# Optimization experiments

Measured on AMD Instinct MI355X. Metric: run time of the kernel, lower is better.

Reference implementation:

```python
import jax, jax.numpy as jnp
import numpy as np

B, S, D, H = 1, 2048, 1024, 16
HD = D // H
FF = 4 * D
EPS_LN = 1e-5
EPS_ATTN = 1e-6


def _layernorm(x, g, b):
    mu = jnp.mean(x, axis=-1, keepdims=True)
    var = jnp.mean(jnp.square(x - mu), axis=-1, keepdims=True)
    return (x - mu) * jax.lax.rsqrt(var + EPS_LN) * g + b


def setup_inputs() -> dict:
    key = jax.random.key(0)
    ks = jax.random.split(key, 12)
    w = lambda k, shape: (jax.random.normal(k, shape, jnp.float32) * 0.02)
    return {
        "x": jax.random.normal(ks[0], (B, S, D), jnp.float32),
        "Wq": w(ks[1], (D, D)), "bq": jnp.zeros((D,), jnp.float32),
        "Wk": w(ks[2], (D, D)), "bk": jnp.zeros((D,), jnp.float32),
        "Wv": w(ks[3], (D, D)), "bv": jnp.zeros((D,), jnp.float32),
        "Wo": w(ks[4], (D, D)), "bo": jnp.zeros((D,), jnp.float32),
        "W1": w(ks[5], (FF, D)), "bb1": jnp.zeros((FF,), jnp.float32),
        "W2": w(ks[6], (D, FF)), "bb2": jnp.zeros((D,), jnp.float32),
        "g1": jnp.ones((D,), jnp.float32), "be1": jnp.zeros((D,), jnp.float32),
        "g2": jnp.ones((D,), jnp.float32), "be2": jnp.zeros((D,), jnp.float32),
    }


def reference(x, Wq, bq, Wk, bk, Wv, bv, Wo, bo, W1, bb1, W2, bb2, g1, be1, g2, be2):
    # --- pre-norm causal linear attention ---
    h = _layernorm(x, g1, be1)                     # (B,S,D)
    def heads(t):
        return t.reshape(B, S, H, HD).transpose(0, 2, 1, 3)  # (B,H,S,hd)
    q = heads(h @ Wq.T + bq)
    k = heads(h @ Wk.T + bk)
    v = heads(h @ Wv.T + bv)
    # feature map phi(x) = elu(x) + 1 (strictly positive)
    q = jax.nn.elu(q) + 1.0
    k = jax.nn.elu(k) + 1.0
    # causal cumulative state: S_t = sum_{i<=t} k_i v_i^T ; z_t = sum_{i<=t} k_i
    kv = jnp.cumsum(jnp.einsum("bhsd,bhse->bhsde", k, v), axis=2)  # (B,H,S,hd,hd)
    z = jnp.cumsum(k, axis=2)                                       # (B,H,S,hd)
    num = jnp.einsum("bhsd,bhsde->bhse", q, kv)                    # (B,H,S,hd)
    den = jnp.einsum("bhsd,bhsd->bhs", q, z) + EPS_ATTN
    attn = (num / den[..., None]).transpose(0, 2, 1, 3).reshape(B, S, D)
    attn = attn @ Wo.T + bo
    x = x + attn
    # --- FFN (GELU exact, matching torch nn.GELU default) ---
    h2 = _layernorm(x, g2, be2)
    ff = jax.nn.gelu(h2 @ W1.T + bb1, approximate=False) @ W2.T + bb2
    return x + ff
```

## Files before the change

kernel.cpp:

```cpp
#include <hip/hip_runtime.h>
#include <hip/hip_bf16.h>
#include <math.h>

constexpr int S  = 2048;
constexpr int D  = 1024;
constexpr int H  = 16;
constexpr int HD = 64;
constexpr int FF = 4096;
constexpr int NC  = 32;
constexpr int CHK = 64;
constexpr int QS  = 3 * D;

typedef __attribute__((ext_vector_type(8))) short bf16x8;
typedef __attribute__((ext_vector_type(4))) float f32x4;
typedef __attribute__((ext_vector_type(16))) float f32x16;

__device__ inline unsigned short f2bf(float f) {
    unsigned int u = __float_as_uint(f);
    u = (u + 0x7FFFu + ((u >> 16) & 1u)) >> 16;
    return (unsigned short)u;
}

constexpr int DD4 = D * D / 4;
constexpr int FD4 = FF * D / 4;
constexpr int CVT_TOTAL4 = 4 * DD4 + 2 * FD4;
constexpr int CVT_BLOCKS = CVT_TOTAL4 / 256;

__global__ __launch_bounds__(256) void cvt_ln(const float* __restrict__ x,
                                              const float* __restrict__ g,
                                              const float* __restrict__ b,
                                              unsigned short* __restrict__ lnout,
                                              const float* __restrict__ Wq,
                                              const float* __restrict__ Wk,
                                              const float* __restrict__ Wv,
                                              const float* __restrict__ Wo,
                                              const float* __restrict__ W1,
                                              const float* __restrict__ W2,
                                              unsigned short* __restrict__ Wqkvb,
                                              unsigned short* __restrict__ Wob,
                                              unsigned short* __restrict__ W1b,
                                              unsigned short* __restrict__ W2b) {
    const int tid = threadIdx.x;
    if (blockIdx.x >= S) {
        int i = (blockIdx.x - S) * 256 + tid;
        const float* s;
        unsigned short* dp;
        if (i < DD4)                 { s = Wq + (size_t)i * 4;               dp = Wqkvb + (size_t)i * 4; }
        else if (i < 2 * DD4)        { s = Wk + (size_t)(i - DD4) * 4;       dp = Wqkvb + (size_t)i * 4; }
        else if (i < 3 * DD4)        { s = Wv + (size_t)(i - 2 * DD4) * 4;   dp = Wqkvb + (size_t)i * 4; }
        else if (i < 4 * DD4)        { s = Wo + (size_t)(i - 3 * DD4) * 4;   dp = Wob + (size_t)(i - 3 * DD4) * 4; }
        else if (i < 4 * DD4 + FD4)  { s = W1 + (size_t)(i - 4 * DD4) * 4;   dp = W1b + (size_t)(i - 4 * DD4) * 4; }
        else                         { s = W2 + (size_t)(i - 4 * DD4 - FD4) * 4; dp = W2b + (size_t)(i - 4 * DD4 - FD4) * 4; }
        float4 v = *(const float4*)s;
        ushort4 o = { f2bf(v.x), f2bf(v.y), f2bf(v.z), f2bf(v.w) };
        *(ushort4*)dp = o;
        return;
    }
    const int row = blockIdx.x;
    float4 v = ((const float4*)(x + (size_t)row * D))[tid];
    float s  = v.x + v.y + v.z + v.w;
    float ss = v.x*v.x + v.y*v.y + v.z*v.z + v.w*v.w;
    #pragma unroll
    for (int off = 32; off > 0; off >>= 1) {
        s  += __shfl_down(s, off);
        ss += __shfl_down(ss, off);
    }
    __shared__ float sw[4], ssw[4];
    if ((tid & 63) == 0) { sw[tid >> 6] = s; ssw[tid >> 6] = ss; }
    __syncthreads();
    s  = sw[0] + sw[1] + sw[2] + sw[3];
    ss = ssw[0] + ssw[1] + ssw[2] + ssw[3];
    const float mu = s * (1.0f / D);
    const float rs = rsqrtf(ss * (1.0f / D) - mu * mu + 1e-5f);
    float4 gv = ((const float4*)g)[tid];
    float4 bv = ((const float4*)b)[tid];
    ushort4 o = { f2bf((v.x - mu) * rs * gv.x + bv.x),
                  f2bf((v.y - mu) * rs * gv.y + bv.y),
                  f2bf((v.z - mu) * rs * gv.z + bv.z),
                  f2bf((v.w - mu) * rs * gv.w + bv.w) };
    ((ushort4*)(lnout + (size_t)row * D))[tid] = o;
}

template <int KS>
__global__ __launch_bounds__(256) void reduce_ln(const float* __restrict__ part,
                                                 const float* __restrict__ bias,
                                                 const float* __restrict__ res,
                                                 float* __restrict__ x2,
                                                 const float* __restrict__ g,
                                                 const float* __restrict__ b,
                                                 unsigned short* __restrict__ out) {
    const int row = blockIdx.x, tid = threadIdx.x;
    const size_t i4 = (size_t)row * 256 + tid;
    float4 a = ((const float4*)part)[i4];
    #pragma unroll
    for (int z = 1; z < KS; ++z) {
        float4 p = ((const float4*)part)[(size_t)z * S * 256 + i4];
        a.x += p.x; a.y += p.y; a.z += p.z; a.w += p.w;
    }
    float4 bi = ((const float4*)bias)[tid];
    float4 r  = ((const float4*)res)[i4];
    a.x += bi.x + r.x; a.y += bi.y + r.y; a.z += bi.z + r.z; a.w += bi.w + r.w;
    ((float4*)x2)[i4] = a;
    float s  = a.x + a.y + a.z + a.w;
    float ss = a.x*a.x + a.y*a.y + a.z*a.z + a.w*a.w;
    #pragma unroll
    for (int off = 32; off > 0; off >>= 1) {
        s  += __shfl_down(s, off);
        ss += __shfl_down(ss, off);
    }
    __shared__ float sw[4], ssw[4];
    if ((tid & 63) == 0) { sw[tid >> 6] = s; ssw[tid >> 6] = ss; }
    __syncthreads();
    s  = sw[0] + sw[1] + sw[2] + sw[3];
    ss = ssw[0] + ssw[1] + ssw[2] + ssw[3];
    const float mu = s * (1.0f / D);
    const float rs = rsqrtf(ss * (1.0f / D) - mu * mu + 1e-5f);
    float4 gv = ((const float4*)g)[tid];
    float4 bv = ((const float4*)b)[tid];
    ushort4 o = { f2bf((a.x - mu) * rs * gv.x + bv.x),
                  f2bf((a.y - mu) * rs * gv.y + bv.y),
                  f2bf((a.z - mu) * rs * gv.z + bv.z),
                  f2bf((a.w - mu) * rs * gv.w + bv.w) };
    ((ushort4*)(out + (size_t)row * D))[tid] = o;
}

enum { EPI_F32 = 0, EPI_QKV = 1, EPI_GELU_BF16 = 2, EPI_PART = 3, EPI_BIAS_RES = 4 };

template <int EPI>
__global__ __launch_bounds__(512, 2) void gemm_bt2(const unsigned short* __restrict__ A,
                                                   const unsigned short* __restrict__ W,
                                                   const float* __restrict__ bias,
                                                   const float* __restrict__ bias2,
                                                   const float* __restrict__ bias3,
                                                   void* __restrict__ outp,
                                                   int M, int N, int K) {
    __shared__ unsigned short As[3][256 * 64];
    __shared__ unsigned short Bs[3][128 * 64];
    const int tid   = threadIdx.x;
    const int tileM = blockIdx.x * 256;
    const int tileN = blockIdx.y * 128;
    const int w    = tid >> 6, lane = tid & 63;
    const int wm   = (w >> 1) * 64, wn = (w & 1) * 64;
    const int l31  = lane & 31, lhi = lane >> 5;
    const int sw32 = (l31 >> 1) & 7;
    const int nt   = K >> 6;

    f32x16 acc[2][2];
    #pragma unroll
    for (int i = 0; i < 2; ++i)
        #pragma unroll
        for (int j = 0; j < 2; ++j) acc[i][j] = (f32x16)(0.0f);

    auto stage = [&](int buf, int k0) {
        #pragma unroll
        for (int p = 0; p < 4; ++p) {
            const int c   = p * 512 + tid;
            const int row = c >> 3;
            const int kc  = (c & 7) ^ ((row >> 1) & 7);
            __builtin_amdgcn_global_load_lds(
                (const __attribute__((address_space(1))) unsigned int*)
                    (A + (size_t)(tileM + row) * K + k0 + kc * 8),
                (__attribute__((address_space(3))) unsigned int*)&As[buf][c * 8],
                16, 0, 0);
        }
        #pragma unroll
        for (int p = 0; p < 2; ++p) {
            const int c   = p * 512 + tid;
            const int row = c >> 3;
            const int kc  = (c & 7) ^ ((row >> 1) & 7);
            __builtin_amdgcn_global_load_lds(
                (const __attribute__((address_space(1))) unsigned int*)
                    (W + (size_t)(tileN + row) * K + k0 + kc * 8),
                (__attribute__((address_space(3))) unsigned int*)&Bs[buf][c * 8],
                16, 0, 0);
        }
    };

    stage(0, 0);
    if (nt > 1) stage(1, 64);

    int k0 = 0;
    for (int t = 0; t < nt; ++t, k0 += 64) {
        if (t + 1 < nt) asm volatile("s_waitcnt vmcnt(6) lgkmcnt(0)" ::: "memory");
        else            asm volatile("s_waitcnt vmcnt(0) lgkmcnt(0)" ::: "memory");
        __builtin_amdgcn_s_barrier();
        if (t + 2 < nt) stage((t + 2) % 3, k0 + 128);

        const unsigned short* Ab = &As[t % 3][0];
        const unsigned short* Bb = &Bs[t % 3][0];
        bf16x8 af[4][2], bfv[4][2];
        #pragma unroll
        for (int s = 0; s < 4; ++s) {
            const int slot = (2 * s + lhi) ^ sw32;
            #pragma unroll
            for (int i = 0; i < 2; ++i)
                af[s][i] = *(const bf16x8*)&Ab[(wm + i * 32 + l31) * 64 + slot * 8];
            #pragma unroll
            for (int j = 0; j < 2; ++j)
                bfv[s][j] = *(const bf16x8*)&Bb[(wn + j * 32 + l31) * 64 + slot * 8];
        }
        __builtin_amdgcn_s_setprio(1);
        #pragma unroll
        for (int s = 0; s < 4; ++s)
            #pragma unroll
            for (int i = 0; i < 2; ++i)
                #pragma unroll
                for (int j = 0; j < 2; ++j)
                    acc[i][j] = __builtin_amdgcn_mfma_f32_32x32x16_bf16(af[s][i], bfv[s][j], acc[i][j], 0, 0, 0);
        __builtin_amdgcn_s_setprio(0);
    }

    #pragma unroll
    for (int i = 0; i < 2; ++i) {
        #pragma unroll
        for (int j = 0; j < 2; ++j) {
            const int col = tileN + wn + j * 32 + l31;
            #pragma unroll
            for (int q = 0; q < 4; ++q) {
                const int rbase = tileM + wm + i * 32 + q * 8 + lhi * 4;
                #pragma unroll
                for (int r = 0; r < 4; ++r) {
                    const int row = rbase + r;
                    const size_t off = (size_t)row * N + col;
                    float v = acc[i][j][q * 4 + r];
                    if constexpr (EPI == EPI_QKV) {
                        float bc = (col < D) ? bias[col] : ((col < 2 * D) ? bias2[col - D] : bias3[col - 2 * D]);
                        v += bc;
                        if (col < 2 * D) v = v > 0.0f ? v + 1.0f : __expf(v);
                        ((float*)outp)[off] = v;
                    } else if constexpr (EPI == EPI_GELU_BF16) {
                        v += bias[col];
                        float gl = 0.5f * v * (1.0f + erff(v * 0.70710678118654752f));
                        ((unsigned short*)outp)[off] = f2bf(gl);
                    } else {
                        v += bias[col];
                        ((float*)outp)[off] = v;
                    }
                }
            }
        }
    }
}

template <int EPI>
__global__ __launch_bounds__(256, 2) void gemm_n64(const unsigned short* __restrict__ A,
                                                   const unsigned short* __restrict__ W,
                                                   const float* __restrict__ bias,
                                                   const float* __restrict__ res,
                                                   void* __restrict__ outp,
                                                   int M, int N, int K) {
    __shared__ unsigned short As[3][128 * 64];
    __shared__ unsigned short Bs[3][64 * 64];
    const int tid   = threadIdx.x;
    const int tileM = blockIdx.x * 128;
    const int tileN = blockIdx.y * 64;
    const int w    = tid >> 6, lane = tid & 63;
    const int wm   = (w >> 1) * 64, wn = (w & 1) * 32;
    const int l31  = lane & 31, lhi = lane >> 5;
    const int sw32 = (l31 >> 1) & 7;
    const int nt   = K >> 6;

    f32x16 acc[2];
    #pragma unroll
    for (int i = 0; i < 2; ++i) acc[i] = (f32x16)(0.0f);

    auto stage = [&](int buf, int k0) {
        #pragma unroll
        for (int p = 0; p < 4; ++p) {
            const int c   = p * 256 + tid;
            const int row = c >> 3;
            const int kc  = (c & 7) ^ ((row >> 1) & 7);
            __builtin_amdgcn_global_load_lds(
                (const __attribute__((address_space(1))) unsigned int*)
                    (A + (size_t)(tileM + row) * K + k0 + kc * 8),
                (__attribute__((address_space(3))) unsigned int*)&As[buf][c * 8],
                16, 0, 0);
        }
        #pragma unroll
        for (int p = 0; p < 2; ++p) {
            const int c   = p * 256 + tid;
            const int row = c >> 3;
            const int kc  = (c & 7) ^ ((row >> 1) & 7);
            __builtin_amdgcn_global_load_lds(
                (const __attribute__((address_space(1))) unsigned int*)
                    (W + (size_t)(tileN + row) * K + k0 + kc * 8),
                (__attribute__((address_space(3))) unsigned int*)&Bs[buf][c * 8],
                16, 0, 0);
        }
    };

    stage(0, 0);
    if (nt > 1) stage(1, 64);

    int k0 = 0;
    for (int t = 0; t < nt; ++t, k0 += 64) {
        if (t + 1 < nt) asm volatile("s_waitcnt vmcnt(6) lgkmcnt(0)" ::: "memory");
        else            asm volatile("s_waitcnt vmcnt(0) lgkmcnt(0)" ::: "memory");
        __builtin_amdgcn_s_barrier();
        if (t + 2 < nt) stage((t + 2) % 3, k0 + 128);

        const unsigned short* Ab = &As[t % 3][0];
        const unsigned short* Bb = &Bs[t % 3][0];
        bf16x8 af[4][2], bfv[4];
        #pragma unroll
        for (int s = 0; s < 4; ++s) {
            const int slot = (2 * s + lhi) ^ sw32;
            #pragma unroll
            for (int i = 0; i < 2; ++i)
                af[s][i] = *(const bf16x8*)&Ab[(wm + i * 32 + l31) * 64 + slot * 8];
            bfv[s] = *(const bf16x8*)&Bb[(wn + l31) * 64 + slot * 8];
        }
        __builtin_amdgcn_s_setprio(1);
        #pragma unroll
        for (int s = 0; s < 4; ++s)
            #pragma unroll
            for (int i = 0; i < 2; ++i)
                acc[i] = __builtin_amdgcn_mfma_f32_32x32x16_bf16(af[s][i], bfv[s], acc[i], 0, 0, 0);
        __builtin_amdgcn_s_setprio(0);
    }

    #pragma unroll
    for (int i = 0; i < 2; ++i) {
        const int col = tileN + wn + l31;
        #pragma unroll
        for (int q = 0; q < 4; ++q) {
            const int rbase = tileM + wm + i * 32 + q * 8 + lhi * 4;
            #pragma unroll
            for (int r = 0; r < 4; ++r) {
                const int row = rbase + r;
                const size_t off = (size_t)row * N + col;
                float v = acc[i][q * 4 + r];
                if constexpr (EPI == EPI_BIAS_RES) {
                    v += bias[col] + res[off];
                    ((float*)outp)[off] = v;
                } else {
                    ((float*)outp)[off] = v;
                }
            }
        }
    }
}

__global__ __launch_bounds__(256) void attn_chunk_sums(const float* __restrict__ qkv,
                                                       float* __restrict__ KVc,
                                                       float* __restrict__ Zc) {
    const int c = blockIdx.x, h = blockIdx.y, tid = threadIdx.x;
    __shared__ float Kc[CHK * HD], Vc[CHK * HD];
    const int s0 = c * CHK;
    #pragma unroll
    for (int p = 0; p < 4; ++p) {
        int cc = p * 256 + tid;
        int t = cc >> 4, dp = (cc & 15) * 4;
        *(float4*)&Kc[t * HD + dp] = *(const float4*)(qkv + (size_t)(s0 + t) * QS + D     + h * HD + dp);
        *(float4*)&Vc[t * HD + dp] = *(const float4*)(qkv + (size_t)(s0 + t) * QS + 2 * D + h * HD + dp);
    }
    __syncthreads();
    const int d = tid >> 2, e0 = (tid & 3) * 16;
    float acc[16];
    #pragma unroll
    for (int j = 0; j < 16; ++j) acc[j] = 0.0f;
    float zacc = 0.0f;
    for (int t = 0; t < CHK; ++t) {
        float kv = Kc[t * HD + d];
        zacc += kv;
        #pragma unroll
        for (int j = 0; j < 16; ++j) acc[j] += kv * Vc[t * HD + e0 + j];
    }
    float* op = KVc + ((size_t)(h * NC + c) * HD + d) * HD + e0;
    #pragma unroll
    for (int j = 0; j < 16; ++j) op[j] = acc[j];
    if ((tid & 3) == 0) Zc[(size_t)(h * NC + c) * HD + d] = zacc;
}

__global__ __launch_bounds__(256) void attn_prefix(float* __restrict__ KVc,
                                                   float* __restrict__ Zc) {
    const int h = blockIdx.y;
    const int elem = blockIdx.x * 256 + threadIdx.x;
    size_t base = (size_t)h * NC * (HD * HD) + elem;
    float v[NC];
    #pragma unroll
    for (int c = 0; c < NC; ++c) v[c] = KVc[base + (size_t)c * (HD * HD)];
    float run = 0.0f;
    #pragma unroll
    for (int c = 0; c < NC; ++c) { float t = v[c]; v[c] = run; run += t; }
    #pragma unroll
    for (int c = 0; c < NC; ++c) KVc[base + (size_t)c * (HD * HD)] = v[c];
    if (blockIdx.x == 0 && threadIdx.x < HD) {
        size_t zb = (size_t)h * NC * HD + threadIdx.x;
        float z[NC];
        #pragma unroll
        for (int c = 0; c < NC; ++c) z[c] = Zc[zb + (size_t)c * HD];
        float zr = 0.0f;
        #pragma unroll
        for (int c = 0; c < NC; ++c) { float t = z[c]; z[c] = zr; zr += t; }
        #pragma unroll
        for (int c = 0; c < NC; ++c) Zc[zb + (size_t)c * HD] = z[c];
    }
}

__global__ __launch_bounds__(256) void attn_out(const float* __restrict__ qkv,
                                                const float* __restrict__ KVpre,
                                                const float* __restrict__ Zpre,
                                                unsigned short* __restrict__ attn) {
    const int c = blockIdx.x, h = blockIdx.y, tid = threadIdx.x;
    __shared__ float Qc[CHK * HD], KVs[CHK * HD], Pre[HD * HD], Sc[CHK * CHK];
    __shared__ float zp[HD], den[CHK];
    const int s0 = c * CHK;
    #pragma unroll
    for (int p = 0; p < 4; ++p) {
        int cc = p * 256 + tid;
        int t = cc >> 4, dp = (cc & 15) * 4;
        *(float4*)&Qc[t * HD + dp]  = *(const float4*)(qkv + (size_t)(s0 + t) * QS +     h * HD + dp);
        *(float4*)&KVs[t * HD + dp] = *(const float4*)(qkv + (size_t)(s0 + t) * QS + D + h * HD + dp);
        ((float4*)Pre)[cc] = *(const float4*)(KVpre + (size_t)(h * NC + c) * (HD * HD) + cc * 4);
    }
    if (tid < HD) zp[tid] = Zpre[(size_t)(h * NC + c) * HD + tid];
    __syncthreads();

    const int tt = tid >> 2, i0 = (tid & 3) * 16;
    for (int i = i0; i < i0 + 16; ++i) {
        float sv = 0.0f;
        for (int d2 = 0; d2 < HD; ++d2) sv += Qc[tt * HD + d2] * KVs[i * HD + d2];
        Sc[tt * CHK + i] = (i <= tt) ? sv : 0.0f;
    }
    __syncthreads();

    if (tid < CHK) {
        float dv = 1e-6f;
        for (int d2 = 0; d2 < HD; ++d2) dv += Qc[tid * HD + d2] * zp[d2];
        for (int i = 0; i < CHK; ++i) dv += Sc[tid * CHK + i];
        den[tid] = dv;
    }
    #pragma unroll
    for (int p = 0; p < 4; ++p) {
        int cc = p * 256 + tid;
        int t = cc >> 4, dp = (cc & 15) * 4;
        *(float4*)&KVs[t * HD + dp] = *(const float4*)(qkv + (size_t)(s0 + t) * QS + 2 * D + h * HD + dp);
    }
    __syncthreads();

    float o[16];
    #pragma unroll
    for (int j = 0; j < 16; ++j) o[j] = 0.0f;
    for (int d2 = 0; d2 < HD; ++d2) {
        float qv = Qc[tt * HD + d2];
        float sv = Sc[tt * CHK + d2];
        #pragma unroll
        for (int j = 0; j < 16; ++j)
            o[j] += qv * Pre[d2 * HD + i0 + j] + sv * KVs[d2 * HD + i0 + j];
    }
    const float inv = 1.0f / den[tt];
    unsigned short* op = attn + (size_t)(s0 + tt) * D + h * HD + i0;
    #pragma unroll
    for (int j0 = 0; j0 < 16; j0 += 4) {
        ushort4 ov = { f2bf(o[j0] * inv), f2bf(o[j0 + 1] * inv),
                       f2bf(o[j0 + 2] * inv), f2bf(o[j0 + 3] * inv) };
        *(ushort4*)(op + j0) = ov;
    }
}

extern "C" void kernel_launch(void* const* d_in, const int* in_sizes, int n_in,
                              void* d_out, int out_size, void* d_ws, size_t ws_size,
                              hipStream_t stream) {
    const float* x   = (const float*)d_in[0];
    const float* Wq  = (const float*)d_in[1];
    const float* bq  = (const float*)d_in[2];
    const float* Wk  = (const float*)d_in[3];
    const float* bk  = (const float*)d_in[4];
    const float* Wv  = (const float*)d_in[5];
    const float* bv  = (const float*)d_in[6];
    const float* Wo  = (const float*)d_in[7];
    const float* bo  = (const float*)d_in[8];
    const float* W1  = (const float*)d_in[9];
    const float* b1  = (const float*)d_in[10];
    const float* W2  = (const float*)d_in[11];
    const float* b2  = (const float*)d_in[12];
    const float* g1  = (const float*)d_in[13];
    const float* be1 = (const float*)d_in[14];
    const float* g2  = (const float*)d_in[15];
    const float* be2 = (const float*)d_in[16];
    float* out = (float*)d_out;

    char* wsp = (char*)d_ws;
    auto alloc = [&](size_t bytes) {
        char* p = wsp;
        wsp += (bytes + 255) & ~(size_t)255;
        return p;
    };
    unsigned short* h1   = (unsigned short*)alloc((size_t)S * D * 2);
    unsigned short* attn = (unsigned short*)alloc((size_t)S * D * 2);
    unsigned short* gbuf = (unsigned short*)alloc((size_t)S * FF * 2);
    float* x2   = (float*)alloc((size_t)S * D * 4);
    unsigned short* Wqkvb = (unsigned short*)alloc((size_t)3 * D * D * 2);
    unsigned short* Wob   = (unsigned short*)alloc((size_t)D * D * 2);
    unsigned short* W1b   = (unsigned short*)alloc((size_t)FF * D * 2);
    unsigned short* W2b   = (unsigned short*)alloc((size_t)D * FF * 2);
    float* KVc  = (float*)alloc((size_t)H * NC * HD * HD * 4);
    float* Zc   = (float*)alloc((size_t)H * NC * HD * 4);
    char* uni = (char*)alloc((size_t)32 * 1024 * 1024);
    float* qkv   = (float*)uni;
    float* parts = (float*)uni;

    cvt_ln<<<S + CVT_BLOCKS, 256, 0, stream>>>(x, g1, be1, h1,
                                               Wq, Wk, Wv, Wo, W1, W2,
                                               Wqkvb, Wob, W1b, W2b);

    gemm_bt2<EPI_QKV><<<dim3(S / 256, 3 * D / 128, 1), 512, 0, stream>>>(
        h1, Wqkvb, bq, bk, bv, qkv, S, 3 * D, D);

    attn_chunk_sums<<<dim3(NC, H), 256, 0, stream>>>(qkv, KVc, Zc);
    attn_prefix<<<dim3(16, H), 256, 0, stream>>>(KVc, Zc);
    attn_out<<<dim3(NC, H), 256, 0, stream>>>(qkv, KVc, Zc, attn);

    gemm_n64<EPI_PART><<<dim3(S / 128, D / 64, 1), 256, 0, stream>>>(
        attn, Wob, nullptr, nullptr, parts, S, D, D);
    reduce_ln<1><<<S, 256, 0, stream>>>(parts, bo, x, x2, g2, be2, h1);

    gemm_bt2<EPI_GELU_BF16><<<dim3(S / 256, FF / 128, 1), 512, 0, stream>>>(
        h1, W1b, b1, nullptr, nullptr, gbuf, S, FF, D);

    gemm_n64<EPI_BIAS_RES><<<dim3(S / 128, D / 64, 1), 256, 0, stream>>>(
        gbuf, W2b, b2, x2, out, S, D, FF);
}
```

Before: 308.9 us.

## Fuse the whole layer into one cooperative persistent megakernel with grid syncs

```diff
diff --git a/kernel.cpp b/kernel.cpp
--- a/kernel.cpp
+++ b/kernel.cpp
@@ -1,6 +1,9 @@
 #include <hip/hip_runtime.h>
+#include <hip/hip_cooperative_groups.h>
 #include <hip/hip_bf16.h>
 #include <math.h>
+
+namespace cg = cooperative_groups;
 
 constexpr int S  = 2048;
 constexpr int D  = 1024;
@@ -11,8 +14,10 @@
 constexpr int CHK = 64;
 constexpr int QS  = 3 * D;
 
+constexpr int NBLK = 256;
+constexpr int NTHR = 512;
+
 typedef __attribute__((ext_vector_type(8))) short bf16x8;
-typedef __attribute__((ext_vector_type(4))) float f32x4;
 typedef __attribute__((ext_vector_type(16))) float f32x16;
 
 __device__ inline unsigned short f2bf(float f) {
@@ -24,126 +29,27 @@
 constexpr int DD4 = D * D / 4;
 constexpr int FD4 = FF * D / 4;
 constexpr int CVT_TOTAL4 = 4 * DD4 + 2 * FD4;
-constexpr int CVT_BLOCKS = CVT_TOTAL4 / 256;
-
-__global__ __launch_bounds__(256) void cvt_ln(const float* __restrict__ x,
-                                              const float* __restrict__ g,
-                                              const float* __restrict__ b,
-                                              unsigned short* __restrict__ lnout,
-                                              const float* __restrict__ Wq,
-                                              const float* __restrict__ Wk,
-                                              const float* __restrict__ Wv,
-                                              const float* __restrict__ Wo,
-                                              const float* __restrict__ W1,
-                                              const float* __restrict__ W2,
-                                              unsigned short* __restrict__ Wqkvb,
-                                              unsigned short* __restrict__ Wob,
-                                              unsigned short* __restrict__ W1b,
-                                              unsigned short* __restrict__ W2b) {
+
+enum { EPI_QKV = 1, EPI_GELU_BF16 = 2, EPI_PART = 3 };
+
+template <int EPI>
+__device__ void gemm_phase(const unsigned short* __restrict__ A,
+                           const unsigned short* __restrict__ W,
+                           const float* __restrict__ bias,
+                           const float* __restrict__ bias2,
+                           const float* __restrict__ bias3,
+                           void* __restrict__ outp,
+                           int M, int N, int K,
+                           int tileM, int tileN, int kStart, int kLen, int zIdx,
+                           unsigned char* sm) {
+    auto As = (unsigned short(*)[256 * 64])(sm);
+    auto Bs = (unsigned short(*)[128 * 64])(sm + 3 * 256 * 64 * 2);
     const int tid = threadIdx.x;
-    if (blockIdx.x >= S) {
-        int i = (blockIdx.x - S) * 256 + tid;
-        const float* s;
-        unsigned short* dp;
-        if (i < DD4)                 { s = Wq + (size_t)i * 4;               dp = Wqkvb + (size_t)i * 4; }
-        else if (i < 2 * DD4)        { s = Wk + (size_t)(i - DD4) * 4;       dp = Wqkvb + (size_t)i * 4; }
-        else if (i < 3 * DD4)        { s = Wv + (size_t)(i - 2 * DD4) * 4;   dp = Wqkvb + (size_t)i * 4; }
-        else if (i < 4 * DD4)        { s = Wo + (size_t)(i - 3 * DD4) * 4;   dp = Wob + (size_t)(i - 3 * DD4) * 4; }
-        else if (i < 4 * DD4 + FD4)  { s = W1 + (size_t)(i - 4 * DD4) * 4;   dp = W1b + (size_t)(i - 4 * DD4) * 4; }
-        else                         { s = W2 + (size_t)(i - 4 * DD4 - FD4) * 4; dp = W2b + (size_t)(i - 4 * DD4 - FD4) * 4; }
-        float4 v = *(const float4*)s;
-        ushort4 o = { f2bf(v.x), f2bf(v.y), f2bf(v.z), f2bf(v.w) };
-        *(ushort4*)dp = o;
-        return;
-    }
-    const int row = blockIdx.x;
-    float4 v = ((const float4*)(x + (size_t)row * D))[tid];
-    float s  = v.x + v.y + v.z + v.w;
-    float ss = v.x*v.x + v.y*v.y + v.z*v.z + v.w*v.w;
-    #pragma unroll
-    for (int off = 32; off > 0; off >>= 1) {
-        s  += __shfl_down(s, off);
-        ss += __shfl_down(ss, off);
-    }
-    __shared__ float sw[4], ssw[4];
-    if ((tid & 63) == 0) { sw[tid >> 6] = s; ssw[tid >> 6] = ss; }
-    __syncthreads();
-    s  = sw[0] + sw[1] + sw[2] + sw[3];
-    ss = ssw[0] + ssw[1] + ssw[2] + ssw[3];
-    const float mu = s * (1.0f / D);
-    const float rs = rsqrtf(ss * (1.0f / D) - mu * mu + 1e-5f);
-    float4 gv = ((const float4*)g)[tid];
-    float4 bv = ((const float4*)b)[tid];
-    ushort4 o = { f2bf((v.x - mu) * rs * gv.x + bv.x),
-                  f2bf((v.y - mu) * rs * gv.y + bv.y),
-                  f2bf((v.z - mu) * rs * gv.z + bv.z),
-                  f2bf((v.w - mu) * rs * gv.w + bv.w) };
-    ((ushort4*)(lnout + (size_t)row * D))[tid] = o;
-}
-
-template <int KS>
-__global__ __launch_bounds__(256) void reduce_ln(const float* __restrict__ part,
-                                                 const float* __restrict__ bias,
-                                                 const float* __restrict__ res,
-                                                 float* __restrict__ x2,
-                                                 const float* __restrict__ g,
-                                                 const float* __restrict__ b,
-                                                 unsigned short* __restrict__ out) {
-    const int row = blockIdx.x, tid = threadIdx.x;
-    const size_t i4 = (size_t)row * 256 + tid;
-    float4 a = ((const float4*)part)[i4];
-    #pragma unroll
-    for (int z = 1; z < KS; ++z) {
-        float4 p = ((const float4*)part)[(size_t)z * S * 256 + i4];
-        a.x += p.x; a.y += p.y; a.z += p.z; a.w += p.w;
-    }
-    float4 bi = ((const float4*)bias)[tid];
-    float4 r  = ((const float4*)res)[i4];
-    a.x += bi.x + r.x; a.y += bi.y + r.y; a.z += bi.z + r.z; a.w += bi.w + r.w;
-    ((float4*)x2)[i4] = a;
-    float s  = a.x + a.y + a.z + a.w;
-    float ss = a.x*a.x + a.y*a.y + a.z*a.z + a.w*a.w;
-    #pragma unroll
-    for (int off = 32; off > 0; off >>= 1) {
-        s  += __shfl_down(s, off);
-        ss += __shfl_down(ss, off);
-    }
-    __shared__ float sw[4], ssw[4];
-    if ((tid & 63) == 0) { sw[tid >> 6] = s; ssw[tid >> 6] = ss; }
-    __syncthreads();
-    s  = sw[0] + sw[1] + sw[2] + sw[3];
-    ss = ssw[0] + ssw[1] + ssw[2] + ssw[3];
-    const float mu = s * (1.0f / D);
-    const float rs = rsqrtf(ss * (1.0f / D) - mu * mu + 1e-5f);
-    float4 gv = ((const float4*)g)[tid];
-    float4 bv = ((const float4*)b)[tid];
-    ushort4 o = { f2bf((a.x - mu) * rs * gv.x + bv.x),
-                  f2bf((a.y - mu) * rs * gv.y + bv.y),
-                  f2bf((a.z - mu) * rs * gv.z + bv.z),
-                  f2bf((a.w - mu) * rs * gv.w + bv.w) };
-    ((ushort4*)(out + (size_t)row * D))[tid] = o;
-}
-
-enum { EPI_F32 = 0, EPI_QKV = 1, EPI_GELU_BF16 = 2, EPI_PART = 3, EPI_BIAS_RES = 4 };
-
-template <int EPI>
-__global__ __launch_bounds__(512, 2) void gemm_bt2(const unsigned short* __restrict__ A,
-                                                   const unsigned short* __restrict__ W,
-                                                   const float* __restrict__ bias,
-                                                   const float* __restrict__ bias2,
-                                                   const float* __restrict__ bias3,
-                                                   void* __restrict__ outp,
-                                                   int M, int N, int K) {
-    __shared__ unsigned short As[3][256 * 64];
-    __shared__ unsigned short Bs[3][128 * 64];
-    const int tid   = threadIdx.x;
-    const int tileM = blockIdx.x * 256;
-    const int tileN = blockIdx.y * 128;
-    const int w    = tid >> 6, lane = tid & 63;
-    const int wm   = (w >> 1) * 64, wn = (w & 1) * 64;
-    const int l31  = lane & 31, lhi = lane >> 5;
+    const int w = tid >> 6, lane = tid & 63;
+    const int wm = (w >> 1) * 64, wn = (w & 1) * 64;
+    const int l31 = lane & 31, lhi = lane >> 5;
     const int sw32 = (l31 >> 1) & 7;
-    const int nt   = K >> 6;
+    const int nt = kLen >> 6;
 
     f32x16 acc[2][2];
     #pragma unroll
@@ -154,9 +60,9 @@
     auto stage = [&](int buf, int k0) {
         #pragma unroll
         for (int p = 0; p < 4; ++p) {
-            const int c   = p * 512 + tid;
+            const int c = p * 512 + tid;
             const int row = c >> 3;
-            const int kc  = (c & 7) ^ ((row >> 1) & 7);
+            const int kc = (c & 7) ^ ((row >> 1) & 7);
             __builtin_amdgcn_global_load_lds(
                 (const __attribute__((address_space(1))) unsigned int*)
                     (A + (size_t)(tileM + row) * K + k0 + kc * 8),
@@ -165,9 +71,9 @@
         }
         #pragma unroll
         for (int p = 0; p < 2; ++p) {
-            const int c   = p * 512 + tid;
+            const int c = p * 512 + tid;
             const int row = c >> 3;
-            const int kc  = (c & 7) ^ ((row >> 1) & 7);
+            const int kc = (c & 7) ^ ((row >> 1) & 7);
             __builtin_amdgcn_global_load_lds(
                 (const __attribute__((address_space(1))) unsigned int*)
                     (W + (size_t)(tileN + row) * K + k0 + kc * 8),
@@ -176,10 +82,10 @@
         }
     };
 
-    stage(0, 0);
-    if (nt > 1) stage(1, 64);
-
-    int k0 = 0;
+    stage(0, kStart);
+    if (nt > 1) stage(1, kStart + 64);
+
+    int k0 = kStart;
     for (int t = 0; t < nt; ++t, k0 += 64) {
         if (t + 1 < nt) asm volatile("s_waitcnt vmcnt(6) lgkmcnt(0)" ::: "memory");
         else            asm volatile("s_waitcnt vmcnt(0) lgkmcnt(0)" ::: "memory");
@@ -223,7 +129,9 @@
                     const int row = rbase + r;
                     const size_t off = (size_t)row * N + col;
                     float v = acc[i][j][q * 4 + r];
-                    if constexpr (EPI == EPI_QKV) {
+                    if constexpr (EPI == EPI_PART) {
+                        ((float*)outp)[(size_t)zIdx * (size_t)M * (size_t)N + off] = v;
+                    } else if constexpr (EPI == EPI_QKV) {
                         float bc = (col < D) ? bias[col] : ((col < 2 * D) ? bias2[col - D] : bias3[col - 2 * D]);
                         v += bc;
                         if (col < 2 * D) v = v > 0.0f ? v + 1.0f : __expf(v);
@@ -232,9 +140,6 @@
                         v += bias[col];
                         float gl = 0.5f * v * (1.0f + erff(v * 0.70710678118654752f));
                         ((unsigned short*)outp)[off] = f2bf(gl);
-                    } else {
-                        v += bias[col];
-                        ((float*)outp)[off] = v;
                     }
                 }
             }
@@ -242,23 +147,18 @@
     }
 }
 
-template <int EPI>
-__global__ __launch_bounds__(256, 2) void gemm_n64(const unsigned short* __restrict__ A,
-                                                   const unsigned short* __restrict__ W,
-                                                   const float* __restrict__ bias,
-                                                   const float* __restrict__ res,
-                                                   void* __restrict__ outp,
-                                                   int M, int N, int K) {
-    __shared__ unsigned short As[3][128 * 64];
-    __shared__ unsigned short Bs[3][64 * 64];
-    const int tid   = threadIdx.x;
-    const int tileM = blockIdx.x * 128;
-    const int tileN = blockIdx.y * 64;
-    const int w    = tid >> 6, lane = tid & 63;
-    const int wm   = (w >> 1) * 64, wn = (w & 1) * 32;
-    const int l31  = lane & 31, lhi = lane >> 5;
+__device__ void n64_phase(const unsigned short* __restrict__ A,
+                          const unsigned short* __restrict__ W,
+                          float* __restrict__ outp,
+                          int M, int N, int K, int tileM, int tileN,
+                          unsigned char* sm, int lt) {
+    auto As = (unsigned short(*)[128 * 64])(sm);
+    auto Bs = (unsigned short(*)[64 * 64])(sm + 3 * 128 * 64 * 2);
+    const int w = lt >> 6, lane = lt & 63;
+    const int wm = (w >> 1) * 64, wn = (w & 1) * 32;
+    const int l31 = lane & 31, lhi = lane >> 5;
     const int sw32 = (l31 >> 1) & 7;
-    const int nt   = K >> 6;
+    const int nt = K >> 6;
 
     f32x16 acc[2];
     #pragma unroll
@@ -267,9 +167,9 @@
     auto stage = [&](int buf, int k0) {
         #pragma unroll
         for (int p = 0; p < 4; ++p) {
-            const int c   = p * 256 + tid;
+            const int c = p * 256 + lt;
             const int row = c >> 3;
-            const int kc  = (c & 7) ^ ((row >> 1) & 7);
+            const int kc = (c & 7) ^ ((row >> 1) & 7);
             __builtin_amdgcn_global_load_lds(
                 (const __attribute__((address_space(1))) unsigned int*)
                     (A + (size_t)(tileM + row) * K + k0 + kc * 8),
@@ -278,9 +178,9 @@
         }
         #pragma unroll
         for (int p = 0; p < 2; ++p) {
-            const int c   = p * 256 + tid;
+            const int c = p * 256 + lt;
             const int row = c >> 3;
-            const int kc  = (c & 7) ^ ((row >> 1) & 7);
+            const int kc = (c & 7) ^ ((row >> 1) & 7);
             __builtin_amdgcn_global_load_lds(
                 (const __attribute__((address_space(1))) unsigned int*)
                     (W + (size_t)(tileN + row) * K + k0 + kc * 8),
@@ -308,7 +208,7 @@
             #pragma unroll
             for (int i = 0; i < 2; ++i)
                 af[s][i] = *(const bf16x8*)&Ab[(wm + i * 32 + l31) * 64 + slot * 8];
-            bfv[s] = *(const bf16x8*)&Bb[(wn + l31) * 64 + slot * 8];
+            bfv[s] = *(const bf16x8*)&Bs[t % 3][(wn + l31) * 64 + slot * 8 - 0];
         }
         __builtin_amdgcn_s_setprio(1);
         #pragma unroll
@@ -328,159 +228,263 @@
             #pragma unroll
             for (int r = 0; r < 4; ++r) {
                 const int row = rbase + r;
-                const size_t off = (size_t)row * N + col;
-                float v = acc[i][q * 4 + r];
-                if constexpr (EPI == EPI_BIAS_RES) {
-                    v += bias[col] + res[off];
-                    ((float*)outp)[off] = v;
-                } else {
-                    ((float*)outp)[off] = v;
-                }
+                outp[(size_t)row * N + col] = acc[i][q * 4 + r];
             }
         }
     }
 }
 
-__global__ __launch_bounds__(256) void attn_chunk_sums(const float* __restrict__ qkv,
-                                                       float* __restrict__ KVc,
-                                                       float* __restrict__ Zc) {
-    const int c = blockIdx.x, h = blockIdx.y, tid = threadIdx.x;
-    __shared__ float Kc[CHK * HD], Vc[CHK * HD];
-    const int s0 = c * CHK;
-    #pragma unroll
-    for (int p = 0; p < 4; ++p) {
-        int cc = p * 256 + tid;
-        int t = cc >> 4, dp = (cc & 15) * 4;
-        *(float4*)&Kc[t * HD + dp] = *(const float4*)(qkv + (size_t)(s0 + t) * QS + D     + h * HD + dp);
-        *(float4*)&Vc[t * HD + dp] = *(const float4*)(qkv + (size_t)(s0 + t) * QS + 2 * D + h * HD + dp);
-    }
-    __syncthreads();
-    const int d = tid >> 2, e0 = (tid & 3) * 16;
-    float acc[16];
-    #pragma unroll
-    for (int j = 0; j < 16; ++j) acc[j] = 0.0f;
-    float zacc = 0.0f;
-    for (int t = 0; t < CHK; ++t) {
-        float kv = Kc[t * HD + d];
-        zacc += kv;
-        #pragma unroll
-        for (int j = 0; j < 16; ++j) acc[j] += kv * Vc[t * HD + e0 + j];
-    }
-    float* op = KVc + ((size_t)(h * NC + c) * HD + d) * HD + e0;
-    #pragma unroll
-    for (int j = 0; j < 16; ++j) op[j] = acc[j];
-    if ((tid & 3) == 0) Zc[(size_t)(h * NC + c) * HD + d] = zacc;
-}
-
-__global__ __launch_bounds__(256) void attn_prefix(float* __restrict__ KVc,
-                                                   float* __restrict__ Zc) {
-    const int h = blockIdx.y;
-    const int elem = blockIdx.x * 256 + threadIdx.x;
-    size_t base = (size_t)h * NC * (HD * HD) + elem;
-    float v[NC];
-    #pragma unroll
-    for (int c = 0; c < NC; ++c) v[c] = KVc[base + (size_t)c * (HD * HD)];
-    float run = 0.0f;
-    #pragma unroll
-    for (int c = 0; c < NC; ++c) { float t = v[c]; v[c] = run; run += t; }
-    #pragma unroll
-    for (int c = 0; c < NC; ++c) KVc[base + (size_t)c * (HD * HD)] = v[c];
-    if (blockIdx.x == 0 && threadIdx.x < HD) {
-        size_t zb = (size_t)h * NC * HD + threadIdx.x;
-        float z[NC];
-        #pragma unroll
-        for (int c = 0; c < NC; ++c) z[c] = Zc[zb + (size_t)c * HD];
-        float zr = 0.0f;
-        #pragma unroll
-        for (int c = 0; c < NC; ++c) { float t = z[c]; z[c] = zr; zr += t; }
-        #pragma unroll
-        for (int c = 0; c < NC; ++c) Zc[zb + (size_t)c * HD] = z[c];
-    }
-}
-
-__global__ __launch_bounds__(256) void attn_out(const float* __restrict__ qkv,
-                                                const float* __restrict__ KVpre,
-                                                const float* __restrict__ Zpre,
-                                                unsigned short* __restrict__ attn) {
-    const int c = blockIdx.x, h = blockIdx.y, tid = threadIdx.x;
-    __shared__ float Qc[CHK * HD], KVs[CHK * HD], Pre[HD * HD], Sc[CHK * CHK];
-    __shared__ float zp[HD], den[CHK];
-    const int s0 = c * CHK;
-    #pragma unroll
-    for (int p = 0; p < 4; ++p) {
-        int cc = p * 256 + tid;
-        int t = cc >> 4, dp = (cc & 15) * 4;
-        *(float4*)&Qc[t * HD + dp]  = *(const float4*)(qkv + (size_t)(s0 + t) * QS +     h * HD + dp);
-        *(float4*)&KVs[t * HD + dp] = *(const float4*)(qkv + (size_t)(s0 + t) * QS + D + h * HD + dp);
-        ((float4*)Pre)[cc] = *(const float4*)(KVpre + (size_t)(h * NC + c) * (HD * HD) + cc * 4);
-    }
-    if (tid < HD) zp[tid] = Zpre[(size_t)(h * NC + c) * HD + tid];
-    __syncthreads();
-
-    const int tt = tid >> 2, i0 = (tid & 3) * 16;
-    for (int i = i0; i < i0 + 16; ++i) {
-        float sv = 0.0f;
-        for (int d2 = 0; d2 < HD; ++d2) sv += Qc[tt * HD + d2] * KVs[i * HD + d2];
-        Sc[tt * CHK + i] = (i <= tt) ? sv : 0.0f;
-    }
-    __syncthreads();
-
-    if (tid < CHK) {
-        float dv = 1e-6f;
-        for (int d2 = 0; d2 < HD; ++d2) dv += Qc[tid * HD + d2] * zp[d2];
-        for (int i = 0; i < CHK; ++i) dv += Sc[tid * CHK + i];
-        den[tid] = dv;
-    }
-    #pragma unroll
-    for (int p = 0; p < 4; ++p) {
-        int cc = p * 256 + tid;
-        int t = cc >> 4, dp = (cc & 15) * 4;
-        *(float4*)&KVs[t * HD + dp] = *(const float4*)(qkv + (size_t)(s0 + t) * QS + 2 * D + h * HD + dp);
-    }
-    __syncthreads();
-
-    float o[16];
-    #pragma unroll
-    for (int j = 0; j < 16; ++j) o[j] = 0.0f;
-    for (int d2 = 0; d2 < HD; ++d2) {
-        float qv = Qc[tt * HD + d2];
-        float sv = Sc[tt * CHK + d2];
-        #pragma unroll
-        for (int j = 0; j < 16; ++j)
-            o[j] += qv * Pre[d2 * HD + i0 + j] + sv * KVs[d2 * HD + i0 + j];
-    }
-    const float inv = 1.0f / den[tt];
-    unsigned short* op = attn + (size_t)(s0 + tt) * D + h * HD + i0;
-    #pragma unroll
-    for (int j0 = 0; j0 < 16; j0 += 4) {
-        ushort4 ov = { f2bf(o[j0] * inv), f2bf(o[j0 + 1] * inv),
-                       f2bf(o[j0 + 2] * inv), f2bf(o[j0 + 3] * inv) };
-        *(ushort4*)(op + j0) = ov;
+struct MegaArgs {
+    const float *x;
+    const float *Wq, *bq, *Wk, *bk, *Wv, *bv, *Wo, *bo, *W1, *b1, *W2, *b2;
+    const float *g1, *be1, *g2, *be2;
+    unsigned short *h1, *attn, *gbuf;
+    float *x2;
+    unsigned short *Wqkvb, *Wob, *W1b, *W2b;
+    float *KVc, *Zc, *uni, *out;
+};
+
+__global__ __launch_bounds__(NTHR, 2) void mega(MegaArgs a) {
+    cg::grid_group grid = cg::this_grid();
+    __shared__ __align__(16) unsigned char SM[147456];
+    const int bid = blockIdx.x, tid = threadIdx.x;
+    const int half = tid >> 8, lt = tid & 255;
+    float* qkv = a.uni;
+    float* parts = a.uni;
+
+    for (int i = bid * NTHR + tid; i < CVT_TOTAL4; i += NBLK * NTHR) {
+        const float* s;
+        unsigned short* dp;
+        if (i < DD4)                 { s = a.Wq + (size_t)i * 4;               dp = a.Wqkvb + (size_t)i * 4; }
+        else if (i < 2 * DD4)        { s = a.Wk + (size_t)(i - DD4) * 4;       dp = a.Wqkvb + (size_t)i * 4; }
+        else if (i < 3 * DD4)        { s = a.Wv + (size_t)(i - 2 * DD4) * 4;   dp = a.Wqkvb + (size_t)i * 4; }
+        else if (i < 4 * DD4)        { s = a.Wo + (size_t)(i - 3 * DD4) * 4;   dp = a.Wob + (size_t)(i - 3 * DD4) * 4; }
+        else if (i < 4 * DD4 + FD4)  { s = a.W1 + (size_t)(i - 4 * DD4) * 4;   dp = a.W1b + (size_t)(i - 4 * DD4) * 4; }
+        else                         { s = a.W2 + (size_t)(i - 4 * DD4 - FD4) * 4; dp = a.W2b + (size_t)(i - 4 * DD4 - FD4) * 4; }
+        float4 v = *(const float4*)s;
+        ushort4 o = { f2bf(v.x), f2bf(v.y), f2bf(v.z), f2bf(v.w) };
+        *(ushort4*)dp = o;
+    }
+    {
+        float* sw = (float*)SM;  float* ssw = sw + 8;
+        for (int r0 = 0; r0 < 8; r0 += 2) {
+            const int row = bid * 8 + r0 + half;
+            float4 v = ((const float4*)(a.x + (size_t)row * D))[lt];
+            float s = v.x + v.y + v.z + v.w;
+            float ss = v.x * v.x + v.y * v.y + v.z * v.z + v.w * v.w;
+            #pragma unroll
+            for (int off = 32; off > 0; off >>= 1) { s += __shfl_down(s, off); ss += __shfl_down(ss, off); }
+            if ((lt & 63) == 0) { sw[half * 4 + (lt >> 6)] = s; ssw[half * 4 + (lt >> 6)] = ss; }
+            __syncthreads();
+            s  = sw[half * 4] + sw[half * 4 + 1] + sw[half * 4 + 2] + sw[half * 4 + 3];
+            ss = ssw[half * 4] + ssw[half * 4 + 1] + ssw[half * 4 + 2] + ssw[half * 4 + 3];
+            const float mu = s * (1.0f / D);
+            const float rs = rsqrtf(ss * (1.0f / D) - mu * mu + 1e-5f);
+            float4 gv = ((const float4*)a.g1)[lt];
+            float4 bv = ((const float4*)a.be1)[lt];
+            ushort4 o = { f2bf((v.x - mu) * rs * gv.x + bv.x), f2bf((v.y - mu) * rs * gv.y + bv.y),
+                          f2bf((v.z - mu) * rs * gv.z + bv.z), f2bf((v.w - mu) * rs * gv.w + bv.w) };
+            ((ushort4*)(a.h1 + (size_t)row * D))[lt] = o;
+            __syncthreads();
+        }
+    }
+    grid.sync();
+
+    if (bid < 192)
+        gemm_phase<EPI_QKV>(a.h1, a.Wqkvb, a.bq, a.bk, a.bv, qkv, S, 3 * D, D,
+                            (bid & 7) * 256, (bid >> 3) * 128, 0, D, 0, SM);
+    grid.sync();
+
+    {
+        const int u = bid * 2 + half, c = u & (NC - 1), h = u >> 5;
+        float* Kc = (float*)(SM + half * 32768);
+        float* Vc = Kc + CHK * HD;
+        const int s0 = c * CHK;
+        #pragma unroll
+        for (int p = 0; p < 4; ++p) {
+            int cc = p * 256 + lt;
+            int t = cc >> 4, dp = (cc & 15) * 4;
+            *(float4*)&Kc[t * HD + dp] = *(const float4*)(qkv + (size_t)(s0 + t) * QS + D + h * HD + dp);
+            *(float4*)&Vc[t * HD + dp] = *(const float4*)(qkv + (size_t)(s0 + t) * QS + 2 * D + h * HD + dp);
+        }
+        __syncthreads();
+        const int d = lt >> 2, e0 = (lt & 3) * 16;
+        float acc[16];
+        #pragma unroll
+        for (int j = 0; j < 16; ++j) acc[j] = 0.0f;
+        float zacc = 0.0f;
+        for (int t = 0; t < CHK; ++t) {
+            float kv = Kc[t * HD + d];
+            zacc += kv;
+            #pragma unroll
+            for (int j = 0; j < 16; ++j) acc[j] += kv * Vc[t * HD + e0 + j];
+        }
+        float* op = a.KVc + ((size_t)(h * NC + c) * HD + d) * HD + e0;
+        #pragma unroll
+        for (int j = 0; j < 16; ++j) op[j] = acc[j];
+        if ((lt & 3) == 0) a.Zc[(size_t)(h * NC + c) * HD + d] = zacc;
+    }
+    grid.sync();
+
+    {
+        const int flat = bid * NTHR + tid;
+        if (flat < H * HD * HD) {
+            const int h = flat >> 12, elem = flat & 4095;
+            size_t base = (size_t)h * NC * (HD * HD) + elem;
+            float v[NC];
+            #pragma unroll
+            for (int c = 0; c < NC; ++c) v[c] = a.KVc[base + (size_t)c * (HD * HD)];
+            float run = 0.0f;
+            #pragma unroll
+            for (int c = 0; c < NC; ++c) { float t = v[c]; v[c] = run; run += t; }
+            #pragma unroll
+            for (int c = 0; c < NC; ++c) a.KVc[base + (size_t)c * (HD * HD)] = v[c];
+        }
+        const int zi = flat - H * HD * HD;
+        if (zi >= 0 && zi < H * HD) {
+            const int h = zi >> 6, d = zi & 63;
+            size_t zb = (size_t)h * NC * HD + d;
+            float z[NC];
+            #pragma unroll
+            for (int c = 0; c < NC; ++c) z[c] = a.Zc[zb + (size_t)c * HD];
+            float zr = 0.0f;
+            #pragma unroll
+            for (int c = 0; c < NC; ++c) { float t = z[c]; z[c] = zr; zr += t; }
+            #pragma unroll
+            for (int c = 0; c < NC; ++c) a.Zc[zb + (size_t)c * HD] = z[c];
+        }
+    }
+    grid.sync();
+
+    {
+        const int u = bid * 2 + half, c = u & (NC - 1), h = u >> 5;
+        float* Qc = (float*)(SM + half * 69888);
+        float* Kv = Qc + 64 * 68;
+        float* Sc = Kv + 64 * 68;
+        float* Pre = Sc + 64 * 68;
+        float* zp = Pre + 4096;
+        float* den = zp + 64;
+        const int s0 = c * CHK;
+        #pragma unroll
+        for (int p = 0; p < 4; ++p) {
+            int cc = p * 256 + lt;
+            int t = cc >> 4, dp = (cc & 15) * 4;
+            *(float4*)&Qc[t * 68 + dp] = *(const float4*)(qkv + (size_t)(s0 + t) * QS + h * HD + dp);
+            *(float4*)&Kv[t * 68 + dp] = *(const float4*)(qkv + (size_t)(s0 + t) * QS + D + h * HD + dp);
+            ((float4*)Pre)[cc] = *(const float4*)(a.KVc + (size_t)(h * NC + c) * (HD * HD) + cc * 4);
+        }
+        if (lt < HD) zp[lt] = a.Zc[(size_t)(h * NC + c) * HD + lt];
+        __syncthreads();
+
+        const int tt = lt >> 2, i0 = (lt & 3) * 16;
+        for (int i = i0; i < i0 + 16; ++i) {
+            float sv = 0.0f;
+            for (int d2 = 0; d2 < HD; ++d2) sv += Qc[tt * 68 + d2] * Kv[i * 68 + d2];
+            Sc[tt * 68 + i] = (i <= tt) ? sv : 0.0f;
+        }
+        __syncthreads();
+
+        if (lt < CHK) {
+            float dv = 1e-6f;
+            for (int d2 = 0; d2 < HD; ++d2) dv += Qc[lt * 68 + d2] * zp[d2];
+            for (int i = 0; i < CHK; ++i) dv += Sc[lt * 68 + i];
+            den[lt] = dv;
+        }
+        #pragma unroll
+        for (int p = 0; p < 4; ++p) {
+            int cc = p * 256 + lt;
+            int t = cc >> 4, dp = (cc & 15) * 4;
+            *(float4*)&Kv[t * 68 + dp] = *(const float4*)(qkv + (size_t)(s0 + t) * QS + 2 * D + h * HD + dp);
+        }
+        __syncthreads();
+
+        float o[16];
+        #pragma unroll
+        for (int j = 0; j < 16; ++j) o[j] = 0.0f;
+        for (int d2 = 0; d2 < HD; ++d2) {
+            float qv = Qc[tt * 68 + d2];
+            float sv = Sc[tt * 68 + d2];
+            #pragma unroll
+            for (int j = 0; j < 16; ++j)
+                o[j] += qv * Pre[d2 * HD + i0 + j] + sv * Kv[d2 * 68 + i0 + j];
+        }
+        const float inv = 1.0f / den[tt];
+        unsigned short* op = a.attn + (size_t)(s0 + tt) * D + h * HD + i0;
+        #pragma unroll
+        for (int j0 = 0; j0 < 16; j0 += 4) {
+            ushort4 ov = { f2bf(o[j0] * inv), f2bf(o[j0 + 1] * inv),
+                           f2bf(o[j0 + 2] * inv), f2bf(o[j0 + 3] * inv) };
+            *(ushort4*)(op + j0) = ov;
+        }
+    }
+    grid.sync();
+
+    if (bid < 128) {
+        const int u = bid * 2 + half;
+        n64_phase(a.attn, a.Wob, parts, S, D, D,
+                  (u & 15) * 128, (u >> 4) * 64, SM + half * 73728, lt);
+    }
+    grid.sync();
+
+    {
+        float* sw = (float*)SM;  float* ssw = sw + 8;
+        for (int r0 = 0; r0 < 8; r0 += 2) {
+            const int row = bid * 8 + r0 + half;
+            const size_t i4 = (size_t)row * 256 + lt;
+            float4 aa = ((const float4*)parts)[i4];
+            float4 bi = ((const float4*)a.bo)[lt];
+            float4 r = ((const float4*)a.x)[i4];
+            aa.x += bi.x + r.x; aa.y += bi.y + r.y; aa.z += bi.z + r.z; aa.w += bi.w + r.w;
+            ((float4*)a.x2)[i4] = aa;
+            float s = aa.x + aa.y + aa.z + aa.w;
+            float ss = aa.x * aa.x + aa.y * aa.y + aa.z * aa.z + aa.w * aa.w;
+            #pragma unroll
+            for (int off = 32; off > 0; off >>= 1) { s += __shfl_down(s, off); ss += __shfl_down(ss, off); }
+            if ((lt & 63) == 0) { sw[half * 4 + (lt >> 6)] = s; ssw[half * 4 + (lt >> 6)] = ss; }
+            __syncthreads();
+            s  = sw[half * 4] + sw[half * 4 + 1] + sw[half * 4 + 2] + sw[half * 4 + 3];
+            ss = ssw[half * 4] + ssw[half * 4 + 1] + ssw[half * 4 + 2] + ssw[half * 4 + 3];
+            const float mu = s * (1.0f / D);
+            const float rs = rsqrtf(ss * (1.0f / D) - mu * mu + 1e-5f);
+            float4 gv = ((const float4*)a.g2)[lt];
+            float4 bv = ((const float4*)a.be2)[lt];
+            ushort4 o = { f2bf((aa.x - mu) * rs * gv.x + bv.x), f2bf((aa.y - mu) * rs * gv.y + bv.y),
+                          f2bf((aa.z - mu) * rs * gv.z + bv.z), f2bf((aa.w - mu) * rs * gv.w + bv.w) };
+            ((ushort4*)(a.h1 + (size_t)row * D))[lt] = o;
+            __syncthreads();
+        }
+    }
+    grid.sync();
+
+    gemm_phase<EPI_GELU_BF16>(a.h1, a.W1b, a.b1, nullptr, nullptr, a.gbuf, S, FF, D,
+                              (bid & 7) * 256, (bid >> 3) * 128, 0, D, 0, SM);
+    grid.sync();
+
+    gemm_phase<EPI_PART>(a.gbuf, a.W2b, nullptr, nullptr, nullptr, parts, S, D, FF,
+                         (bid & 7) * 256, ((bid >> 3) & 7) * 128, (bid >> 6) * 1024,
+                         1024, bid >> 6, SM);
+    grid.sync();
+
+    {
+        const int total4 = S * D / 4;
+        for (int i = bid * NTHR + tid; i < total4; i += NBLK * NTHR) {
+            float4 aa = ((const float4*)parts)[i];
+            #pragma unroll
+            for (int z = 1; z < 4; ++z) {
+                float4 p = ((const float4*)parts)[(size_t)z * total4 + i];
+                aa.x += p.x; aa.y += p.y; aa.z += p.z; aa.w += p.w;
+            }
+            float4 b = ((const float4*)a.b2)[i & 255];
+            float4 r = ((const float4*)a.x2)[i];
+            aa.x += b.x + r.x; aa.y += b.y + r.y; aa.z += b.z + r.z; aa.w += b.w + r.w;
+            ((float4*)a.out)[i] = aa;
+        }
     }
 }
 
 extern "C" void kernel_launch(void* const* d_in, const int* in_sizes, int n_in,
                               void* d_out, int out_size, void* d_ws, size_t ws_size,
                               hipStream_t stream) {
-    const float* x   = (const float*)d_in[0];
-    const float* Wq  = (const float*)d_in[1];
-    const float* bq  = (const float*)d_in[2];
-    const float* Wk  = (const float*)d_in[3];
-    const float* bk  = (const float*)d_in[4];
-    const float* Wv  = (const float*)d_in[5];
-    const float* bv  = (const float*)d_in[6];
-    const float* Wo  = (const float*)d_in[7];
-    const float* bo  = (const float*)d_in[8];
-    const float* W1  = (const float*)d_in[9];
-    const float* b1  = (const float*)d_in[10];
-    const float* W2  = (const float*)d_in[11];
-    const float* b2  = (const float*)d_in[12];
-    const float* g1  = (const float*)d_in[13];
-    const float* be1 = (const float*)d_in[14];
-    const float* g2  = (const float*)d_in[15];
-    const float* be2 = (const float*)d_in[16];
-    float* out = (float*)d_out;
-
     char* wsp = (char*)d_ws;
     auto alloc = [&](size_t bytes) {
         char* p = wsp;
@@ -490,35 +494,30 @@
     unsigned short* h1   = (unsigned short*)alloc((size_t)S * D * 2);
     unsigned short* attn = (unsigned short*)alloc((size_t)S * D * 2);
     unsigned short* gbuf = (unsigned short*)alloc((size_t)S * FF * 2);
-    float* x2   = (float*)alloc((size_t)S * D * 4);
+    float* x2 = (float*)alloc((size_t)S * D * 4);
     unsigned short* Wqkvb = (unsigned short*)alloc((size_t)3 * D * D * 2);
     unsigned short* Wob   = (unsigned short*)alloc((size_t)D * D * 2);
     unsigned short* W1b   = (unsigned short*)alloc((size_t)FF * D * 2);
     unsigned short* W2b   = (unsigned short*)alloc((size_t)D * FF * 2);
-    float* KVc  = (float*)alloc((size_t)H * NC * HD * HD * 4);
-    float* Zc   = (float*)alloc((size_t)H * NC * HD * 4);
-    char* uni = (char*)alloc((size_t)32 * 1024 * 1024);
-    float* qkv   = (float*)uni;
-    float* parts = (float*)uni;
-
-    cvt_ln<<<S + CVT_BLOCKS, 256, 0, stream>>>(x, g1, be1, h1,
-                                               Wq, Wk, Wv, Wo, W1, W2,
-                                               Wqkvb, Wob, W1b, W2b);
-
-    gemm_bt2<EPI_QKV><<<dim3(S / 256, 3 * D / 128, 1), 512, 0, stream>>>(
-        h1, Wqkvb, bq, bk, bv, qkv, S, 3 * D, D);
-
-    attn_chunk_sums<<<dim3(NC, H), 256, 0, stream>>>(qkv, KVc, Zc);
-    attn_prefix<<<dim3(16, H), 256, 0, stream>>>(KVc, Zc);
-    attn_out<<<dim3(NC, H), 256, 0, stream>>>(qkv, KVc, Zc, attn);
-
-    gemm_n64<EPI_PART><<<dim3(S / 128, D / 64, 1), 256, 0, stream>>>(
-        attn, Wob, nullptr, nullptr, parts, S, D, D);
-    reduce_ln<1><<<S, 256, 0, stream>>>(parts, bo, x, x2, g2, be2, h1);
-
-    gemm_bt2<EPI_GELU_BF16><<<dim3(S / 256, FF / 128, 1), 512, 0, stream>>>(
-        h1, W1b, b1, nullptr, nullptr, gbuf, S, FF, D);
-
-    gemm_n64<EPI_BIAS_RES><<<dim3(S / 128, D / 64, 1), 256, 0, stream>>>(
-        gbuf, W2b, b2, x2, out, S, D, FF);
+    float* KVc = (float*)alloc((size_t)H * NC * HD * HD * 4);
+    float* Zc  = (float*)alloc((size_t)H * NC * HD * 4);
+    float* uni = (float*)alloc((size_t)32 * 1024 * 1024);
+
+    MegaArgs a;
+    a.x   = (const float*)d_in[0];
+    a.Wq  = (const float*)d_in[1];  a.bq  = (const float*)d_in[2];
+    a.Wk  = (const float*)d_in[3];  a.bk  = (const float*)d_in[4];
+    a.Wv  = (const float*)d_in[5];  a.bv  = (const float*)d_in[6];
+    a.Wo  = (const float*)d_in[7];  a.bo  = (const float*)d_in[8];
+    a.W1  = (const float*)d_in[9];  a.b1  = (const float*)d_in[10];
+    a.W2  = (const float*)d_in[11]; a.b2  = (const float*)d_in[12];
+    a.g1  = (const float*)d_in[13]; a.be1 = (const float*)d_in[14];
+    a.g2  = (const float*)d_in[15]; a.be2 = (const float*)d_in[16];
+    a.h1 = h1; a.attn = attn; a.gbuf = gbuf; a.x2 = x2;
+    a.Wqkvb = Wqkvb; a.Wob = Wob; a.W1b = W1b; a.W2b = W2b;
+    a.KVc = KVc; a.Zc = Zc; a.uni = uni; a.out = (float*)d_out;
+
+    void* kargs[] = { &a };
+    hipLaunchCooperativeKernel((const void*)mega, dim3(NBLK), dim3(NTHR),
+                               kargs, 0, stream);
 }
```

New measurement: 578.3 us. 87.2% more time.
